# Performance work log

Measured on AMD Instinct MI355X. Metric: run time of the kernel, lower is better.

## Reference

```python
import jax, jax.numpy as jnp
import numpy as np
from math import sqrt

BASE = 10000.0  # rope_theta
NUM_HEADS = 16


def _quant(x):
    # per-row (last-dim) symmetric int8 fake-quant, matching ActivationQuantSTE.forward
    scale = 127.0 / jnp.maximum(jnp.max(jnp.abs(x), axis=-1, keepdims=True), 1e-5)
    return jnp.clip(jnp.round(x * scale), -128.0, 127.0) / scale


@jax.custom_vjp
def act_quant(x):
    return _quant(x)

def _aq_fwd(x):
    return _quant(x), None

def _aq_bwd(_, g):
    return (g,)  # straight-through estimator

act_quant.defvjp(_aq_fwd, _aq_bwd)


def complex_linear(xr, xi, Wr, Wi):
    # ComplexLinearBase: quantize activations, then
    #   y_real = q_real @ Wr^T + q_imag @ Wi^T
    #   y_imag = q_real @ Wi^T - q_imag @ Wr^T
    qr = act_quant(xr)
    qi = act_quant(xi)
    yr = qr @ Wr.T + qi @ Wi.T
    yi = qr @ Wi.T - qi @ Wr.T
    return yr, yi


def setup_inputs() -> dict:
    T, H = 2048, 2048
    key = jax.random.key(0)
    ks = jax.random.split(key, 10)
    w = lambda k: jax.random.normal(k, (H, H), jnp.float32) * 0.02
    return {
        "hidden_real": jax.random.normal(ks[0], (T, H), jnp.float32),
        "hidden_imag": jax.random.normal(ks[1], (T, H), jnp.float32),
        "positions": jnp.arange(T, dtype=jnp.int32),
        "Wq_r": w(ks[2]), "Wq_i": w(ks[3]),
        "Wk_r": w(ks[4]), "Wk_i": w(ks[5]),
        "Wv_r": w(ks[6]), "Wv_i": w(ks[7]),
        "Wo_r": w(ks[8]), "Wo_i": w(ks[9]),
    }


def reference(hidden_real, hidden_imag, positions, Wq_r, Wq_i, Wk_r, Wk_i, Wv_r, Wv_i, Wo_r, Wo_i):
    T, H = hidden_real.shape
    NH = NUM_HEADS
    D = H // NH  # head_dim

    # complex QKV projections with int8 activation fake-quant
    qr, qi = complex_linear(hidden_real, hidden_imag, Wq_r, Wq_i)
    kr, ki = complex_linear(hidden_real, hidden_imag, Wk_r, Wk_i)
    vr, vi = complex_linear(hidden_real, hidden_imag, Wv_r, Wv_i)

    # Complex RoPE: interleaving (real, imag) then GPT-J-style rotation with
    # head_size = rotary_dim = 2*D is equivalent to rotating (real, imag) pairs:
    #   out_real = real*cos - imag*sin ; out_imag = imag*cos + real*sin
    # inv_freq = base^-(arange(0, 2D, 2)/(2D)) = base^-(arange(D)/D), len D.
    inv_freq = 1.0 / (BASE ** (jnp.arange(D, dtype=jnp.float32) / D))
    freqs = positions.astype(jnp.float32)[:, None] * inv_freq[None, :]  # [T, D]
    # cache is stored in bf16 in the original module
    cos = jnp.cos(freqs).astype(jnp.bfloat16).astype(jnp.float32)[:, None, :]  # [T,1,D]
    sin = jnp.sin(freqs).astype(jnp.bfloat16).astype(jnp.float32)[:, None, :]

    def rope(xr_, xi_):
        r = xr_.reshape(T, NH, D)
        i = xi_.reshape(T, NH, D)
        return r * cos - i * sin, i * cos + r * sin

    qr3, qi3 = rope(qr, qi)
    kr3, ki3 = rope(kr, ki)
    vr3 = vr.reshape(T, NH, D)
    vi3 = vi.reshape(T, NH, D)

    # causal attention; scores = Re(q . conj(k)) / sqrt(2*D)  (complex dim is 2*D)
    scale = 1.0 / sqrt(2 * D)
    scores = (jnp.einsum('thd,shd->hts', qr3, kr3)
              + jnp.einsum('thd,shd->hts', qi3, ki3)) * scale  # [NH, T, T]
    causal = jnp.tril(jnp.ones((T, T), dtype=bool))
    scores = jnp.where(causal[None], scores, -1e9)
    p = jax.nn.softmax(scores, axis=-1)

    out_r = jnp.einsum('hts,shd->thd', p, vr3).reshape(T, H)
    out_i = jnp.einsum('hts,shd->thd', p, vi3).reshape(T, H)

    # complex output projection (with activation fake-quant)
    return complex_linear(out_r, out_i, Wo_r, Wo_i)
```

## Files before the change

kernel.cpp:

```cpp
#include <hip/hip_runtime.h>


typedef float v4f __attribute__((ext_vector_type(4)));
typedef _Float16 v8h __attribute__((ext_vector_type(8)));
typedef _Float16 v4h __attribute__((ext_vector_type(4)));

typedef const __attribute__((address_space(1))) void glob_void;
typedef __attribute__((address_space(3))) void lds_void;

__device__ __forceinline__ void gload16(const _Float16* gp, _Float16* lp) {
  __builtin_amdgcn_global_load_lds((glob_void*)gp, (lds_void*)lp, 16, 0, 0);
}

__device__ __forceinline__ float bf16_rt(float f) {
  union { float f; unsigned u; } a; a.f = f;
  unsigned r = (a.u + 0x7fffu + ((a.u >> 16) & 1u)) & 0xffff0000u;
  union { unsigned u; float f; } b; b.u = r;
  return b.f;
}

#define EPI_QKV 0
#define EPI_OUT 1

template<int EPI>
__global__ __launch_bounds__(256) void gemm_nt(
    const _Float16* __restrict__ A, const _Float16* __restrict__ B,
    void* __restrict__ Cv, int K, int lda, int ldb, int ldc,
    _Float16* __restrict__ vtout)
{
  const int m0 = blockIdx.x * 128, n0 = blockIdx.y * 128;

  __shared__ __align__(16) _Float16 As[128 * 32];
  __shared__ __align__(16) _Float16 Bs[128 * 32];

  const int tid = threadIdx.x, lane = tid & 63, wave = tid >> 6;
  const int off0 = tid * 8, off1 = 2048 + tid * 8;
  const int r0 = off0 >> 5, r1 = off1 >> 5;
  const int c0 = ((((off0 >> 3) & 3) ^ ((r0 >> 1) & 3)) << 3);
  const int c1 = ((((off1 >> 3) & 3) ^ ((r1 >> 1) & 3)) << 3);
  const _Float16* ga0 = A + (long long)(m0 + r0) * lda + c0;
  const _Float16* ga1 = A + (long long)(m0 + r1) * lda + c1;
  const _Float16* gb0 = B + (long long)(n0 + r0) * ldb + c0;
  const _Float16* gb1 = B + (long long)(n0 + r1) * ldb + c1;

  const int mr = (wave >> 1) * 64 + (lane & 15);
  const int nr = (wave & 1) * 64 + (lane & 15);
  const int kq = lane >> 4;

  v4f acc[4][4] = {};

  for (int k0 = 0; k0 < K; k0 += 32) {
    gload16(ga0 + k0, As + off0);
    gload16(ga1 + k0, As + off1);
    gload16(gb0 + k0, Bs + off0);
    gload16(gb1 + k0, Bs + off1);
    __syncthreads();
    v8h a[4], b[4];
#pragma unroll
    for (int i = 0; i < 4; ++i) {
      const int r = mr + i * 16;
      a[i] = *(const v8h*)&As[r * 32 + ((kq ^ ((r >> 1) & 3)) << 3)];
    }
#pragma unroll
    for (int j = 0; j < 4; ++j) {
      const int r = nr + j * 16;
      b[j] = *(const v8h*)&Bs[r * 32 + ((kq ^ ((r >> 1) & 3)) << 3)];
    }
#pragma unroll
    for (int i = 0; i < 4; ++i)
#pragma unroll
      for (int j = 0; j < 4; ++j)
        acc[i][j] = __builtin_amdgcn_mfma_f32_16x16x32_f16(a[i], b[j], acc[i][j], 0, 0, 0);
    __syncthreads();
  }

  const int cr = (wave >> 1) * 64 + (lane >> 4) * 4;
  const int cc = (wave & 1) * 64 + (lane & 15);
#pragma unroll
  for (int i = 0; i < 4; ++i)
#pragma unroll
    for (int j = 0; j < 4; ++j) {
      const int col = n0 + cc + j * 16;
      if (EPI == EPI_QKV && col >= 8192) {
        const int c = col - 8192;
        const int hh = (c & 2047) >> 7;
        const int dcol = (c < 2048) ? (c & 127) : (128 + (c & 127));
        const int row0 = m0 + cr + i * 16;
        v4h p;
#pragma unroll
        for (int r = 0; r < 4; ++r) p[r] = (_Float16)acc[i][j][r];
        *(v4h*)(vtout + ((long long)(hh * 256 + dcol)) * 2048 + row0) = p;
      } else {
#pragma unroll
        for (int r = 0; r < 4; ++r) {
          const int row = m0 + cr + i * 16 + r;
          const float v = acc[i][j][r];
          if (EPI == EPI_QKV) {
            ((_Float16*)Cv)[(long long)row * ldc + col] = (_Float16)v;
          } else {
            float* O = (float*)Cv;
            if (col < 2048) O[(long long)row * 2048 + col] = v;
            else O[2048ll * 2048 + (long long)row * 2048 + (col - 2048)] = v;
          }
        }
      }
    }
}

__global__ __launch_bounds__(256) void quant_rows(
    const float* __restrict__ s0, const float* __restrict__ s1,
    _Float16* __restrict__ dst)
{
  const int t = blockIdx.x, y = blockIdx.y;
  const float* src = (y ? s1 : s0) + (long long)t * 2048;
  const int tid = threadIdx.x, lane = tid & 63, wave = tid >> 6;
  __shared__ float rbuf[4];
  const v4f a = *(const v4f*)(src + tid * 4);
  const v4f b = *(const v4f*)(src + 1024 + tid * 4);
  float m = 0.f;
#pragma unroll
  for (int k = 0; k < 4; ++k)
    m = fmaxf(m, fmaxf(fabsf(a[k]), fabsf(b[k])));
  for (int o = 1; o < 64; o <<= 1) m = fmaxf(m, __shfl_xor(m, o, 64));
  if (lane == 0) rbuf[wave] = m;
  __syncthreads();
  m = fmaxf(fmaxf(rbuf[0], rbuf[1]), fmaxf(rbuf[2], rbuf[3]));
  const float scale = 127.f / fmaxf(m, 1e-5f);
  const float inv = 1.f / scale;
  _Float16* d = dst + (long long)t * 4096 + (long long)y * 2048 + tid * 4;
  v4h qa, qb;
#pragma unroll
  for (int k = 0; k < 4; ++k) {
    qa[k] = (_Float16)(fminf(fmaxf(rintf(a[k] * scale), -128.f), 127.f) * inv);
    qb[k] = (_Float16)(fminf(fmaxf(rintf(b[k] * scale), -128.f), 127.f) * inv);
  }
  *(v4h*)d = qa;
  *(v4h*)(d + 1024) = qb;
}

__global__ __launch_bounds__(256) void wprep(
    const float* __restrict__ Wq_r, const float* __restrict__ Wq_i,
    const float* __restrict__ Wk_r, const float* __restrict__ Wk_i,
    const float* __restrict__ Wv_r, const float* __restrict__ Wv_i,
    const float* __restrict__ Wo_r, const float* __restrict__ Wo_i,
    _Float16* __restrict__ Bqkv, _Float16* __restrict__ Bo)
{
  const float* Ws[8] = {Wq_r, Wq_i, Wk_r, Wk_i, Wv_r, Wv_i, Wo_r, Wo_i};
  const int i = blockIdx.x * 256 + threadIdx.x;
  const int w = i >> 18;
  const int rem = i & 262143;
  const int j = rem >> 7;
  const int cb = (rem & 127) * 16;
  const float* src = Ws[w] + (long long)j * 2048 + cb;
  _Float16* Bp = (w < 6) ? (Bqkv + (long long)(w >> 1) * 4096 * 4096) : Bo;
  const int isI = w & 1;
  _Float16* d1 = Bp + (long long)j * 4096 + (isI ? 2048 + cb : cb);
  _Float16* d2 = Bp + (long long)(2048 + j) * 4096 + (isI ? cb : 2048 + cb);
  const float sg2 = isI ? 1.f : -1.f;
#pragma unroll
  for (int q = 0; q < 4; ++q) {
    const v4f v = *(const v4f*)(src + q * 4);
    v4h o1, o2;
#pragma unroll
    for (int k = 0; k < 4; ++k) {
      o1[k] = (_Float16)v[k];
      o2[k] = (_Float16)(v[k] * sg2);
    }
    *(v4h*)(d1 + q * 4) = o1;
    *(v4h*)(d2 + q * 4) = o2;
  }
}

__global__ __launch_bounds__(256) void trig_kernel(
    const int* __restrict__ pos, float* __restrict__ cs)
{
  const int t = blockIdx.x * 2 + (threadIdx.x >> 7);
  const int d = threadIdx.x & 127;
  const float invf = (float)pow(10000.0, -(double)d / 128.0);
  const float fr = (float)pos[t] * invf;
  const double fd = (double)fr;
  cs[((long long)t * 128 + d) * 2]     = bf16_rt((float)cos(fd));
  cs[((long long)t * 128 + d) * 2 + 1] = bf16_rt((float)sin(fd));
}

__global__ __launch_bounds__(256) void rope_kernel(
    const _Float16* __restrict__ Yq, const float* __restrict__ cs,
    _Float16* __restrict__ qc, _Float16* __restrict__ kc)
{
  const int idx = blockIdx.x * 256 + threadIdx.x;
  const int d0 = (idx & 15) * 8;
  const int h  = (idx >> 4) & 15;
  const int t  = idx >> 8;
  const _Float16* y = Yq + (long long)t * 8192 + h * 128 + d0;
  const v8h qr8 = *(const v8h*)(y);
  const v8h qi8 = *(const v8h*)(y + 2048);
  const v8h kr8 = *(const v8h*)(y + 4096);
  const v8h ki8 = *(const v8h*)(y + 6144);
  const float* cp = cs + ((long long)t * 128 + d0) * 2;
  v8h qro, qio, kro, kio;
#pragma unroll
  for (int u = 0; u < 8; ++u) {
    const float c = cp[u * 2], s = cp[u * 2 + 1];
    const float qr = (float)qr8[u], qi = (float)qi8[u];
    const float kr = (float)kr8[u], ki = (float)ki8[u];
    qro[u] = (_Float16)(qr * c - qi * s);
    qio[u] = (_Float16)(qi * c + qr * s);
    kro[u] = (_Float16)(kr * c - ki * s);
    kio[u] = (_Float16)(ki * c + kr * s);
  }
  _Float16* qo = qc + ((long long)h * 2048 + t) * 256 + d0;
  _Float16* ko = kc + ((long long)h * 2048 + t) * 256 + d0;
  *(v8h*)qo = qro; *(v8h*)(qo + 128) = qio;
  *(v8h*)ko = kro; *(v8h*)(ko + 128) = kio;
}

__global__ __launch_bounds__(256, 2) void flash_attn(
    const _Float16* __restrict__ qc, const _Float16* __restrict__ kc,
    const _Float16* __restrict__ vt, float* __restrict__ attn)
{
  __shared__ __align__(16) _Float16 Ps[64 * 72];
  __shared__ float pmax[2][64];
  __shared__ float psum[2][64];

  const int h  = blockIdx.y;
  const int qt = ((h >> 3) & 1) ? (31 - (int)blockIdx.x) : (int)blockIdx.x;
  const int q0 = qt * 64;
  const int tid = threadIdx.x, lane = tid & 63, wave = tid >> 6;
  const int mi = wave >> 1, ni = wave & 1;
  const int quad = lane >> 4, l15 = lane & 15;

  const _Float16* qh = qc + (long long)h * 2048 * 256;
  const _Float16* kh = kc + (long long)h * 2048 * 256;
  const _Float16* vh = vt + (long long)h * 256 * 2048;

  const _Float16 scl = (_Float16)0.09016844f;
  v8h qf[2][8];
#pragma unroll
  for (int mt = 0; mt < 2; ++mt) {
    const int t = q0 + mi * 32 + mt * 16 + l15;
#pragma unroll
    for (int ks = 0; ks < 8; ++ks) {
      v8h q = *(const v8h*)(qh + (long long)t * 256 + ks * 32 + quad * 8);
#pragma unroll
      for (int u = 0; u < 8; ++u) q[u] *= scl;
      qf[mt][ks] = q;
    }
  }

  float mrow[2][4], lrow[2][4];
  v4f acc_o[2][8];
#pragma unroll
  for (int mt = 0; mt < 2; ++mt)
#pragma unroll
    for (int r = 0; r < 4; ++r) { mrow[mt][r] = -1e30f; lrow[mt][r] = 0.f; }
#pragma unroll
  for (int mt = 0; mt < 2; ++mt)
#pragma unroll
    for (int nt = 0; nt < 8; ++nt) acc_o[mt][nt] = (v4f){0.f, 0.f, 0.f, 0.f};

  for (int st = 0; st <= qt; ++st) {
    const int s0 = st * 64;

    v4f sa[2][2] = {};
#pragma unroll
    for (int ks = 0; ks < 8; ++ks) {
      v8h bk[2];
#pragma unroll
      for (int jn = 0; jn < 2; ++jn)
        bk[jn] = *(const v8h*)(kh + (long long)(s0 + ni * 32 + jn * 16 + l15) * 256
                               + ks * 32 + quad * 8);
#pragma unroll
      for (int mt = 0; mt < 2; ++mt)
#pragma unroll
        for (int jn = 0; jn < 2; ++jn)
          sa[mt][jn] = __builtin_amdgcn_mfma_f32_16x16x32_f16(qf[mt][ks], bk[jn], sa[mt][jn], 0, 0, 0);
    }

    const bool diag = (st == qt);
    float pm[2][4];
#pragma unroll
    for (int mt = 0; mt < 2; ++mt)
#pragma unroll
      for (int r = 0; r < 4; ++r) pm[mt][r] = -1e30f;
#pragma unroll
    for (int mt = 0; mt < 2; ++mt)
#pragma unroll
      for (int jn = 0; jn < 2; ++jn)
#pragma unroll
        for (int r = 0; r < 4; ++r) {
          float v = sa[mt][jn][r];
          if (diag) {
            const int rl = mi * 32 + mt * 16 + quad * 4 + r;
            const int cl = ni * 32 + jn * 16 + l15;
            if (cl > rl) v = -1e30f;
          }
          sa[mt][jn][r] = v;
          pm[mt][r] = fmaxf(pm[mt][r], v);
        }
#pragma unroll
    for (int o = 1; o < 16; o <<= 1)
#pragma unroll
      for (int mt = 0; mt < 2; ++mt)
#pragma unroll
        for (int r = 0; r < 4; ++r)
          pm[mt][r] = fmaxf(pm[mt][r], __shfl_xor(pm[mt][r], o, 64));
    if (l15 == 0) {
#pragma unroll
      for (int mt = 0; mt < 2; ++mt)
#pragma unroll
        for (int r = 0; r < 4; ++r)
          pmax[ni][mi * 32 + mt * 16 + quad * 4 + r] = pm[mt][r];
    }
    __syncthreads();

    float al[2][4], ps[2][4];
#pragma unroll
    for (int mt = 0; mt < 2; ++mt)
#pragma unroll
      for (int r = 0; r < 4; ++r) {
        const int row = mi * 32 + mt * 16 + quad * 4 + r;
        const float mn = fmaxf(mrow[mt][r], fmaxf(pmax[0][row], pmax[1][row]));
        al[mt][r] = __builtin_amdgcn_exp2f(mrow[mt][r] - mn);
        mrow[mt][r] = mn;
        ps[mt][r] = 0.f;
      }
#pragma unroll
    for (int mt = 0; mt < 2; ++mt)
#pragma unroll
      for (int jn = 0; jn < 2; ++jn)
#pragma unroll
        for (int r = 0; r < 4; ++r) {
          const float e = __builtin_amdgcn_exp2f(sa[mt][jn][r] - mrow[mt][r]);
          ps[mt][r] += e;
          Ps[(mi * 32 + mt * 16 + quad * 4 + r) * 72 + ni * 32 + jn * 16 + l15] = (_Float16)e;
        }
#pragma unroll
    for (int o = 1; o < 16; o <<= 1)
#pragma unroll
      for (int mt = 0; mt < 2; ++mt)
#pragma unroll
        for (int r = 0; r < 4; ++r)
          ps[mt][r] += __shfl_xor(ps[mt][r], o, 64);
    if (l15 == 0) {
#pragma unroll
      for (int mt = 0; mt < 2; ++mt)
#pragma unroll
        for (int r = 0; r < 4; ++r)
          psum[ni][mi * 32 + mt * 16 + quad * 4 + r] = ps[mt][r];
    }
    __syncthreads();

#pragma unroll
    for (int mt = 0; mt < 2; ++mt)
#pragma unroll
      for (int r = 0; r < 4; ++r) {
        const int row = mi * 32 + mt * 16 + quad * 4 + r;
        lrow[mt][r] = lrow[mt][r] * al[mt][r] + psum[0][row] + psum[1][row];
      }
#pragma unroll
    for (int mt = 0; mt < 2; ++mt)
#pragma unroll
      for (int nt = 0; nt < 8; ++nt)
#pragma unroll
        for (int r = 0; r < 4; ++r)
          acc_o[mt][nt][r] *= al[mt][r];

#pragma unroll
    for (int kc2 = 0; kc2 < 2; ++kc2) {
      v8h pa[2];
#pragma unroll
      for (int mt = 0; mt < 2; ++mt) {
        const int row = mi * 32 + mt * 16 + l15;
        pa[mt] = *(const v8h*)(Ps + row * 72 + kc2 * 32 + quad * 8);
      }
#pragma unroll
      for (int nt = 0; nt < 8; ++nt) {
        const v8h vb = *(const v8h*)(vh + (long long)(ni * 128 + nt * 16 + l15) * 2048
                                     + s0 + kc2 * 32 + quad * 8);
#pragma unroll
        for (int mt = 0; mt < 2; ++mt)
          acc_o[mt][nt] = __builtin_amdgcn_mfma_f32_16x16x32_f16(pa[mt], vb, acc_o[mt][nt], 0, 0, 0);
      }
    }
  }

#pragma unroll
  for (int mt = 0; mt < 2; ++mt) {
    float inv[4];
#pragma unroll
    for (int r = 0; r < 4; ++r) inv[r] = 1.f / lrow[mt][r];
#pragma unroll
    for (int nt = 0; nt < 8; ++nt) {
      const int d = ni * 128 + nt * 16 + l15;
      float* dst = attn + ((d < 128) ? 0ll : (2048ll * 2048)) + (h * 128 + (d & 127));
#pragma unroll
      for (int r = 0; r < 4; ++r) {
        const int t = q0 + mi * 32 + mt * 16 + quad * 4 + r;
        dst[(long long)t * 2048] = acc_o[mt][nt][r] * inv[r];
      }
    }
  }
}

extern "C" void kernel_launch(void* const* d_in, const int* in_sizes, int n_in,
                              void* d_out, int out_size, void* d_ws, size_t ws_size,
                              hipStream_t stream) {
  const float* hr   = (const float*)d_in[0];
  const float* hi   = (const float*)d_in[1];
  const int*   pos  = (const int*)d_in[2];
  const float* Wq_r = (const float*)d_in[3];
  const float* Wq_i = (const float*)d_in[4];
  const float* Wk_r = (const float*)d_in[5];
  const float* Wk_i = (const float*)d_in[6];
  const float* Wv_r = (const float*)d_in[7];
  const float* Wv_i = (const float*)d_in[8];
  const float* Wo_r = (const float*)d_in[9];
  const float* Wo_i = (const float*)d_in[10];

  char* ws = (char*)d_ws;
  _Float16* Bqkv = (_Float16*)(ws);
  float*    attn = (float*)   (ws);
  float*    cs   = (float*)   (ws + (32ll  << 20));
  _Float16* Bo   = (_Float16*)(ws + (96ll  << 20));
  _Float16* Ac   = (_Float16*)(ws + (128ll << 20));
  _Float16* Yq   = (_Float16*)(ws + (144ll << 20));
  _Float16* qc   = (_Float16*)(ws + (176ll << 20));
  _Float16* kc   = (_Float16*)(ws + (192ll << 20));
  _Float16* vt   = (_Float16*)(ws + (208ll << 20));

  quant_rows<<<dim3(2048, 2), 256, 0, stream>>>(hr, hi, Ac);
  wprep<<<8192, 256, 0, stream>>>(Wq_r, Wq_i, Wk_r, Wk_i, Wv_r, Wv_i, Wo_r, Wo_i, Bqkv, Bo);
  gemm_nt<EPI_QKV><<<dim3(16, 96), 256, 0, stream>>>(
      Ac, Bqkv, Yq, 4096, 4096, 4096, 8192, vt);
  trig_kernel<<<1024, 256, 0, stream>>>(pos, cs);
  rope_kernel<<<2048, 256, 0, stream>>>(Yq, cs, qc, kc);
  flash_attn<<<dim3(32, 16), 256, 0, stream>>>(qc, kc, vt, attn);
  quant_rows<<<dim3(2048, 2), 256, 0, stream>>>(attn, attn + 2048ll * 2048, Ac);
  gemm_nt<EPI_OUT><<<dim3(16, 32), 256, 0, stream>>>(
      Ac, Bo, d_out, 4096, 4096, 4096, 0, nullptr);
}
```

Before: 789.0 us.

## Replace QKV GEMM with 256x192-tile double-buffered 512-thread kernel

```diff
diff --git a/kernel.cpp b/kernel.cpp
--- a/kernel.cpp
+++ b/kernel.cpp
@@ -21,6 +21,115 @@
 
 #define EPI_QKV 0
 #define EPI_OUT 1
+
+__global__ __launch_bounds__(512, 2) void gemm_qkv256(
+    const _Float16* __restrict__ A, const _Float16* __restrict__ B,
+    _Float16* __restrict__ Yq, _Float16* __restrict__ vt)
+{
+  const int p = blockIdx.x;
+  const int xcd = p & 7, s = p >> 3;
+  const int mt = s & 7, ntl = s >> 3;
+  const int nt = xcd * 8 + ntl;
+  const int m0 = mt << 8;
+  const int n0 = nt * 192;
+
+  __shared__ __align__(16) _Float16 lds[57344];
+
+  const int tid = threadIdx.x, lane = tid & 63, wave = tid >> 6;
+  const int quad = lane >> 4, l15 = lane & 15;
+  const int wm = wave >> 2, wn = wave & 3;
+
+  const int rr = tid >> 2;
+  const int lc8 = (((tid & 3) ^ ((tid >> 3) & 3)) << 3);
+  const _Float16* gA = A + (long long)(m0 + rr) * 4096 + lc8;
+  const _Float16* gBj[3];
+#pragma unroll
+  for (int j = 0; j < 3; ++j) {
+    const int ks = (j == 2) || (j == 1 && tid >= 256);
+    const int r = j * 128 + (tid >> 2) - ks * 192;
+    gBj[j] = B + (long long)(n0 + r) * 4096 + ks * 32 + lc8;
+  }
+
+  const int co = ((quad ^ ((l15 >> 1) & 3)) << 3);
+  const int aBase = (wm * 128 + l15) * 32 + co;
+  const int bBase = (wn * 48 + l15) * 32 + co;
+
+  v4f acc[8][3] = {};
+
+  auto stage = [&](int b, int k0) {
+    _Float16* dst = lds + b * 28672 + tid * 8;
+#pragma unroll
+    for (int j = 0; j < 4; ++j)
+      gload16(gA + k0 + (j & 1) * (128 * 4096) + ((j >> 1) << 5), dst + j * 4096);
+#pragma unroll
+    for (int j = 0; j < 3; ++j)
+      gload16(gBj[j] + k0, dst + 16384 + j * 4096);
+  };
+
+  stage(0, 0);
+
+  for (int t = 0; t < 64; ++t) {
+    const int buf = t & 1;
+    __builtin_amdgcn_s_barrier();
+    if (t < 63) {
+      stage(buf ^ 1, (t + 1) << 6);
+      asm volatile("s_waitcnt vmcnt(7)" ::: "memory");
+    } else {
+      asm volatile("s_waitcnt vmcnt(0)" ::: "memory");
+    }
+    __builtin_amdgcn_s_barrier();
+
+    const _Float16* As = lds + buf * 28672;
+    const _Float16* Bs = As + 16384;
+    v8h bf[3][2];
+#pragma unroll
+    for (int nf = 0; nf < 3; ++nf)
+#pragma unroll
+      for (int ks = 0; ks < 2; ++ks)
+        bf[nf][ks] = *(const v8h*)&Bs[bBase + ks * 6144 + nf * 512];
+#pragma unroll
+    for (int mh = 0; mh < 2; ++mh) {
+      v8h af[4][2];
+#pragma unroll
+      for (int i = 0; i < 4; ++i)
+#pragma unroll
+        for (int ks = 0; ks < 2; ++ks)
+          af[i][ks] = *(const v8h*)&As[aBase + ks * 8192 + (mh * 4 + i) * 512];
+      __builtin_amdgcn_s_setprio(1);
+#pragma unroll
+      for (int i = 0; i < 4; ++i)
+#pragma unroll
+        for (int nf = 0; nf < 3; ++nf)
+#pragma unroll
+          for (int ks = 0; ks < 2; ++ks)
+            acc[mh * 4 + i][nf] = __builtin_amdgcn_mfma_f32_16x16x32_f16(
+                af[i][ks], bf[nf][ks], acc[mh * 4 + i][nf], 0, 0, 0);
+      __builtin_amdgcn_s_setprio(0);
+    }
+  }
+
+#pragma unroll
+  for (int mf = 0; mf < 8; ++mf) {
+#pragma unroll
+    for (int nf = 0; nf < 3; ++nf) {
+      const int col = n0 + wn * 48 + nf * 16 + l15;
+      const int row0 = m0 + wm * 128 + mf * 16 + quad * 4;
+      if (col >= 8192) {
+        const int c = col - 8192;
+        const int hh = (c & 2047) >> 7;
+        const int dcol = (c < 2048) ? (c & 127) : (128 + (c & 127));
+        v4h pk;
+#pragma unroll
+        for (int r = 0; r < 4; ++r) pk[r] = (_Float16)acc[mf][nf][r];
+        *(v4h*)(vt + ((long long)(hh * 256 + dcol)) * 2048 + row0) = pk;
+      } else {
+#pragma unroll
+        for (int r = 0; r < 4; ++r)
+          Yq[(long long)(row0 + r) * 8192 + col] = (_Float16)acc[mf][nf][r];
+      }
+    }
+  }
+}
 
 template<int EPI>
 __global__ __launch_bounds__(256) void gemm_nt(
@@ -86,10 +195,10 @@
         const int hh = (c & 2047) >> 7;
         const int dcol = (c < 2048) ? (c & 127) : (128 + (c & 127));
         const int row0 = m0 + cr + i * 16;
-        v4h p;
-#pragma unroll
-        for (int r = 0; r < 4; ++r) p[r] = (_Float16)acc[i][j][r];
-        *(v4h*)(vtout + ((long long)(hh * 256 + dcol)) * 2048 + row0) = p;
+        v4h pk;
+#pragma unroll
+        for (int r = 0; r < 4; ++r) pk[r] = (_Float16)acc[i][j][r];
+        *(v4h*)(vtout + ((long long)(hh * 256 + dcol)) * 2048 + row0) = pk;
       } else {
 #pragma unroll
         for (int r = 0; r < 4; ++r) {
@@ -430,8 +539,7 @@
 
   quant_rows<<<dim3(2048, 2), 256, 0, stream>>>(hr, hi, Ac);
   wprep<<<8192, 256, 0, stream>>>(Wq_r, Wq_i, Wk_r, Wk_i, Wv_r, Wv_i, Wo_r, Wo_i, Bqkv, Bo);
-  gemm_nt<EPI_QKV><<<dim3(16, 96), 256, 0, stream>>>(
-      Ac, Bqkv, Yq, 4096, 4096, 4096, 8192, vt);
+  gemm_qkv256<<<512, 512, 0, stream>>>(Ac, Bqkv, Yq, vt);
   trig_kernel<<<1024, 256, 0, stream>>>(pos, cs);
   rope_kernel<<<2048, 256, 0, stream>>>(Yq, cs, qc, kc);
   flash_attn<<<dim3(32, 16), 256, 0, stream>>>(qc, kc, vt, attn);
```

After: 735.0 us. 1.07x faster.
